# Optimization experiments

Measured on AMD Instinct MI355X. Metric: run time of the kernel, lower is better.

## Reference

```python
import jax, jax.numpy as jnp
import numpy as np

N_NODES = 10000
N_EDGES = 640000
IN_FEATS = 128
HIDDEN = 128
N_CLASSES = 64
EPS = 0.0


def _linear_params(key, fan_in, fan_out):
    k1, k2 = jax.random.split(key)
    bound = 1.0 / np.sqrt(fan_in)
    W = jax.random.uniform(k1, (fan_in, fan_out), jnp.float32, -bound, bound)
    b = jax.random.uniform(k2, (fan_out,), jnp.float32, -bound, bound)
    return W, b


def setup_inputs() -> dict:
    key = jax.random.key(0)
    ks = jax.random.split(key, 8)
    features = jax.random.normal(ks[0], (N_NODES, IN_FEATS), jnp.float32)
    src = jax.random.randint(ks[1], (N_EDGES,), 0, N_NODES, jnp.int64 if jax.config.jax_enable_x64 else jnp.int32)
    dst = jax.random.randint(ks[2], (N_EDGES,), 0, N_NODES, jnp.int64 if jax.config.jax_enable_x64 else jnp.int32)
    W1, b1 = _linear_params(ks[3], IN_FEATS, HIDDEN)
    W3, b3 = _linear_params(ks[4], HIDDEN, HIDDEN)
    W4, b4 = _linear_params(ks[5], HIDDEN, HIDDEN)
    W2, b2 = _linear_params(ks[6], HIDDEN, N_CLASSES)
    return {"features": features, "src": src, "dst": dst,
            "W1": W1, "b1": b1, "W3": W3, "b3": b3,
            "W4": W4, "b4": b4, "W2": W2, "b2": b2}


def gin_conv(h, src, dst, W, b):
    # sum-aggregate neighbor features: agg[v] = sum_{(u->v)} h[u]
    agg = jax.ops.segment_sum(h[src], dst, num_segments=N_NODES)
    z = (1.0 + EPS) * h + agg
    return z @ W + b


def reference(features, src, dst, W1, b1, W3, b3, W4, b4, W2, b2):
    h = gin_conv(features, src, dst, W1, b1)
    h = jax.nn.relu(h)
    h = gin_conv(h, src, dst, W3, b3)
    h = jax.nn.relu(h)
    h = gin_conv(h, src, dst, W4, b4)
    h = jax.nn.relu(h)
    h = gin_conv(h, src, dst, W2, b2)
    return h
```

## Files before the change

kernel.cpp:

```cpp
#include <hip/hip_runtime.h>
#include <hip/hip_bf16.h>

#define N_NODES 10000
#define N_EDGES 640000
#define FEATS   128
#define CAP     192
#define NBUCK   157
#define ECHUNK  2048
#define NPB     313
#define OSTR    160
#define TILE    8


__global__ __launch_bounds__(256) void bin_pack(const int* __restrict__ src,
                                                const int* __restrict__ dst,
                                                uint* __restrict__ bucketed,
                                                ushort* __restrict__ goffs) {
    __shared__ int hist[NBUCK];
    __shared__ int offs[NBUCK + 1];
    __shared__ int scan[256];
    __shared__ uint staging[ECHUNK];
    const int tid = threadIdx.x;
    const int b = blockIdx.x;
    const int e0 = b * ECHUNK;
    for (int i = tid; i < NBUCK; i += 256) hist[i] = 0;
    __syncthreads();
    int dreg[8];
#pragma unroll
    for (int i = 0; i < 8; ++i) {
        int e = e0 + tid + i * 256;
        dreg[i] = (e < N_EDGES) ? dst[e] : -1;
        if (dreg[i] >= 0) atomicAdd(&hist[dreg[i] >> 6], 1);
    }
    __syncthreads();
    int val = (tid < NBUCK) ? hist[tid] : 0;
    scan[tid] = val;
    __syncthreads();
    for (int off = 1; off < 256; off <<= 1) {
        int t = (tid >= off) ? scan[tid - off] : 0;
        __syncthreads();
        scan[tid] += t;
        __syncthreads();
    }
    if (tid < NBUCK) offs[tid] = scan[tid] - val;
    if (tid == 0) offs[NBUCK] = scan[NBUCK - 1];
    for (int i = tid; i < NBUCK; i += 256) hist[i] = 0;
    __syncthreads();
    if (tid <= NBUCK) goffs[b * OSTR + tid] = (ushort)offs[tid];
#pragma unroll
    for (int i = 0; i < 8; ++i) {
        int e = e0 + tid + i * 256;
        if (dreg[i] >= 0) {
            int s = src[e];
            int bk = dreg[i] >> 6;
            int slot = offs[bk] + atomicAdd(&hist[bk], 1);
            staging[slot] = ((uint)s << 6) | (uint)(dreg[i] & 63);
        }
    }
    __syncthreads();
    uint4* gu = (uint4*)(bucketed + (size_t)b * ECHUNK);
    const uint4* lu = (const uint4*)staging;
#pragma unroll
    for (int i = 0; i < ECHUNK / 4 / 256; ++i)
        gu[tid + i * 256] = lu[tid + i * 256];
}


__global__ __launch_bounds__(256) void build_ell(const uint* __restrict__ bucketed,
                                                 const ushort* __restrict__ goffs,
                                                 ushort* __restrict__ ell,
                                                 int* __restrict__ cnts) {
    __shared__ ushort lell[64 * CAP];
    __shared__ int lcur[64];
    const int tid = threadIdx.x;
    const int bk = blockIdx.x;
    if (tid < 64) lcur[tid] = 0;
    __syncthreads();
    for (int b = tid; b < NPB; b += 256) {
        int off0 = goffs[b * OSTR + bk];
        int off1 = goffs[b * OSTR + bk + 1];
        const uint* p0 = bucketed + (size_t)b * ECHUNK;
        for (int i = off0; i < off1; ++i) {
            uint p = p0[i];
            int v = p & 63;
            int slot = atomicAdd(&lcur[v], 1);
            if (slot < CAP) lell[v * CAP + slot] = (ushort)(p >> 6);
        }
    }
    __syncthreads();
    const int node0 = bk * 64;
    int nn = N_NODES - node0;
    if (nn > 64) nn = 64;
    const uint4* lu = (const uint4*)lell;
    uint4* gu = (uint4*)(ell + (size_t)node0 * CAP);
    const int nq = nn * (CAP / 8);
    for (int i = tid; i < nq; i += 256) gu[i] = lu[i];
    for (int v = tid; v < nn; v += 256) {
        int c = lcur[v];
        cnts[node0 + v] = (c > CAP) ? CAP : c;
    }
}


__global__ __launch_bounds__(256) void f2b_kernel(const float* __restrict__ in,
                                                  ushort* __restrict__ out, int n4) {
    int i = blockIdx.x * 256 + threadIdx.x;
    if (i >= n4) return;
    float4 f = ((const float4*)in)[i];
    __hip_bfloat16 b0 = __float2bfloat16(f.x);
    __hip_bfloat16 b1 = __float2bfloat16(f.y);
    __hip_bfloat16 b2 = __float2bfloat16(f.z);
    __hip_bfloat16 b3 = __float2bfloat16(f.w);
    ushort4 o;
    o.x = *(const ushort*)&b0; o.y = *(const ushort*)&b1;
    o.z = *(const ushort*)&b2; o.w = *(const ushort*)&b3;
    ((ushort4*)out)[i] = o;
}


__device__ __forceinline__ float bflo(uint p) { return __uint_as_float(p << 16); }
__device__ __forceinline__ float bfhi(uint p) { return __uint_as_float(p & 0xffff0000u); }

template <int FO, int RELU, int LAST>
__global__ __launch_bounds__(256) void fused_kernel(const ushort* __restrict__ hb,
                                                    const float* __restrict__ W,
                                                    const float* __restrict__ bias,
                                                    const int* __restrict__ cnts,
                                                    const ushort* __restrict__ ell,
                                                    ushort* __restrict__ hb_out,
                                                    float* __restrict__ f_out) {
    __shared__ float sZ[TILE][132];
    const int tile0 = blockIdx.x * TILE;
    const int tid = threadIdx.x;
    const int lane = tid & 63;
    const int wv = tid >> 6;
    const int g = lane >> 4;
    const int q = lane & 15;
    const uint4* __restrict__ hbq = (const uint4*)hb;

#pragma unroll
    for (int n = 0; n < 2; ++n) {
        const int v = tile0 + wv * 2 + n;
        int cnt = cnts[v];
        if (cnt > CAP) cnt = CAP;
        const ushort* __restrict__ row = ell + (size_t)v * CAP;
        float acc[8];
#pragma unroll
        for (int i = 0; i < 8; ++i) acc[i] = 0.f;
#pragma unroll 2
        for (int j = 0; j < cnt; j += 4) {
            uint2 iv = *(const uint2*)(row + j);
            uint word = (g & 2) ? iv.y : iv.x;
            uint u = (g & 1) ? (word >> 16) : (word & 0xffffu);
            float scale = (j + g < cnt) ? 1.0f : 0.0f;
            if (u > N_NODES - 1) u = N_NODES - 1;
            uint4 p = hbq[u * 16 + q];
            acc[0] = fmaf(bflo(p.x), scale, acc[0]);
            acc[1] = fmaf(bfhi(p.x), scale, acc[1]);
            acc[2] = fmaf(bflo(p.y), scale, acc[2]);
            acc[3] = fmaf(bfhi(p.y), scale, acc[3]);
            acc[4] = fmaf(bflo(p.z), scale, acc[4]);
            acc[5] = fmaf(bfhi(p.z), scale, acc[5]);
            acc[6] = fmaf(bflo(p.w), scale, acc[6]);
            acc[7] = fmaf(bfhi(p.w), scale, acc[7]);
        }
#pragma unroll
        for (int d = 16; d < 64; d <<= 1) {
#pragma unroll
            for (int i = 0; i < 8; ++i) acc[i] += __shfl_xor(acc[i], d);
        }
        if (g == 0) {
            uint4 p = hbq[(size_t)v * 16 + q];
            acc[0] += bflo(p.x); acc[1] += bfhi(p.x);
            acc[2] += bflo(p.y); acc[3] += bfhi(p.y);
            acc[4] += bflo(p.z); acc[5] += bfhi(p.z);
            acc[6] += bflo(p.w); acc[7] += bfhi(p.w);
            float4 a0 = {acc[0], acc[1], acc[2], acc[3]};
            float4 a1 = {acc[4], acc[5], acc[6], acc[7]};
            *(float4*)&sZ[wv * 2 + n][q * 8]     = a0;
            *(float4*)&sZ[wv * 2 + n][q * 8 + 4] = a1;
        }
    }
    __syncthreads();

    constexpr int GROUPS = 256 / FO;
    constexpr int ROWS   = TILE / GROUPS;
    const int col = tid % FO;
    const int gg  = tid / FO;
    float acc2[ROWS];
#pragma unroll
    for (int r = 0; r < ROWS; ++r) acc2[r] = 0.f;
#pragma unroll 2
    for (int k = 0; k < 128; k += 4) {
        float w0 = W[(k + 0) * FO + col];
        float w1 = W[(k + 1) * FO + col];
        float w2 = W[(k + 2) * FO + col];
        float w3 = W[(k + 3) * FO + col];
#pragma unroll
        for (int r = 0; r < ROWS; ++r) {
            float4 z = *(const float4*)&sZ[gg * ROWS + r][k];
            acc2[r] = fmaf(z.x, w0, acc2[r]);
            acc2[r] = fmaf(z.y, w1, acc2[r]);
            acc2[r] = fmaf(z.z, w2, acc2[r]);
            acc2[r] = fmaf(z.w, w3, acc2[r]);
        }
    }
    const float b = bias[col];
#pragma unroll
    for (int r = 0; r < ROWS; ++r) {
        const int vv = tile0 + gg * ROWS + r;
        float y = acc2[r] + b;
        if (RELU) y = fmaxf(y, 0.f);
        if (LAST) {
            f_out[(size_t)vv * FO + col] = y;
        } else {
            __hip_bfloat16 bv = __float2bfloat16(y);
            hb_out[(size_t)vv * FEATS + col] = *(const ushort*)&bv;
        }
    }
}


extern "C" void kernel_launch(void* const* d_in, const int* in_sizes, int n_in,
                              void* d_out, int out_size, void* d_ws, size_t ws_size,
                              hipStream_t stream) {
    const float* features = (const float*)d_in[0];
    const int*   src      = (const int*)d_in[1];
    const int*   dst      = (const int*)d_in[2];
    const float* W1 = (const float*)d_in[3];
    const float* b1 = (const float*)d_in[4];
    const float* W3 = (const float*)d_in[5];
    const float* b3 = (const float*)d_in[6];
    const float* W4 = (const float*)d_in[7];
    const float* b4 = (const float*)d_in[8];
    const float* W2 = (const float*)d_in[9];
    const float* b2 = (const float*)d_in[10];
    float* out = (float*)d_out;

    int*    cnts     = (int*)d_ws;
    ushort* goffs    = (ushort*)(cnts + 10240);
    uint*   bucketed = (uint*)(goffs + 50240);
    ushort* ell      = (ushort*)(bucketed + (size_t)NPB * ECHUNK);
    ushort* hb0      = ell + (size_t)N_NODES * CAP;
    ushort* hb1      = hb0 + (size_t)N_NODES * FEATS;

    bin_pack<<<NPB, 256, 0, stream>>>(src, dst, bucketed, goffs);
    build_ell<<<NBUCK, 256, 0, stream>>>(bucketed, goffs, ell, cnts);
    f2b_kernel<<<(N_NODES * FEATS / 4 + 255) / 256, 256, 0, stream>>>(features, hb0, N_NODES * FEATS / 4);

    const int fblocks = N_NODES / TILE;

    fused_kernel<128, 1, 0><<<fblocks, 256, 0, stream>>>(hb0, W1, b1, cnts, ell, hb1, nullptr);
    fused_kernel<128, 1, 0><<<fblocks, 256, 0, stream>>>(hb1, W3, b3, cnts, ell, hb0, nullptr);
    fused_kernel<128, 1, 0><<<fblocks, 256, 0, stream>>>(hb0, W4, b4, cnts, ell, hb1, nullptr);
    fused_kernel<64, 0, 1><<<fblocks, 256, 0, stream>>>(hb1, W2, b2, cnts, ell, nullptr, out);
}
```

Baseline: 120.7 us.

## Reorder last GIN layer as transform-then-aggregate, fold conversion into bin_pack, widen build_ell

The last layer now multiplies by W2 first, producing a 64-wide bf16 intermediate, and then aggregates neighbors in that narrower space, which halves the gather bytes for that layer. The float-to-bf16 feature conversion is merged into bin_pack to save a launch, and build_ell now uses 512 threads with wave-parallel scanning of each bucket. The trade-offs are an extra launch for the split final layer and an extra bf16 rounding of the intermediate before aggregation.

```diff
diff --git a/kernel.cpp b/kernel.cpp
--- a/kernel.cpp
+++ b/kernel.cpp
@@ -11,11 +11,16 @@
 #define OSTR    160
 #define TILE    8
 
+__device__ __forceinline__ float bflo(uint p) { return __uint_as_float(p << 16); }
+__device__ __forceinline__ float bfhi(uint p) { return __uint_as_float(p & 0xffff0000u); }
+
 
 __global__ __launch_bounds__(256) void bin_pack(const int* __restrict__ src,
                                                 const int* __restrict__ dst,
                                                 uint* __restrict__ bucketed,
-                                                ushort* __restrict__ goffs) {
+                                                ushort* __restrict__ goffs,
+                                                const float* __restrict__ features,
+                                                ushort* __restrict__ hb0) {
     __shared__ int hist[NBUCK];
     __shared__ int offs[NBUCK + 1];
     __shared__ int scan[256];
@@ -63,10 +68,23 @@
 #pragma unroll
     for (int i = 0; i < ECHUNK / 4 / 256; ++i)
         gu[tid + i * 256] = lu[tid + i * 256];
-}
-
-
-__global__ __launch_bounds__(256) void build_ell(const uint* __restrict__ bucketed,
+
+    const int n4 = N_NODES * FEATS / 4;
+    for (int i = b * 256 + tid; i < n4; i += NPB * 256) {
+        float4 f = ((const float4*)features)[i];
+        __hip_bfloat16 b0 = __float2bfloat16(f.x);
+        __hip_bfloat16 b1 = __float2bfloat16(f.y);
+        __hip_bfloat16 b2 = __float2bfloat16(f.z);
+        __hip_bfloat16 b3 = __float2bfloat16(f.w);
+        ushort4 o;
+        o.x = *(const ushort*)&b0; o.y = *(const ushort*)&b1;
+        o.z = *(const ushort*)&b2; o.w = *(const ushort*)&b3;
+        ((ushort4*)hb0)[i] = o;
+    }
+}
+
+
+__global__ __launch_bounds__(512) void build_ell(const uint* __restrict__ bucketed,
                                                  const ushort* __restrict__ goffs,
                                                  ushort* __restrict__ ell,
                                                  int* __restrict__ cnts) {
@@ -76,11 +94,13 @@
     const int bk = blockIdx.x;
     if (tid < 64) lcur[tid] = 0;
     __syncthreads();
-    for (int b = tid; b < NPB; b += 256) {
+    const int wv = tid >> 6;
+    const int lane = tid & 63;
+    for (int b = wv; b < NPB; b += 8) {
         int off0 = goffs[b * OSTR + bk];
         int off1 = goffs[b * OSTR + bk + 1];
         const uint* p0 = bucketed + (size_t)b * ECHUNK;
-        for (int i = off0; i < off1; ++i) {
+        for (int i = off0 + lane; i < off1; i += 64) {
             uint p = p0[i];
             int v = p & 63;
             int slot = atomicAdd(&lcur[v], 1);
@@ -94,41 +114,21 @@
     const uint4* lu = (const uint4*)lell;
     uint4* gu = (uint4*)(ell + (size_t)node0 * CAP);
     const int nq = nn * (CAP / 8);
-    for (int i = tid; i < nq; i += 256) gu[i] = lu[i];
-    for (int v = tid; v < nn; v += 256) {
+    for (int i = tid; i < nq; i += 512) gu[i] = lu[i];
+    for (int v = tid; v < nn; v += 512) {
         int c = lcur[v];
         cnts[node0 + v] = (c > CAP) ? CAP : c;
     }
 }
 
 
-__global__ __launch_bounds__(256) void f2b_kernel(const float* __restrict__ in,
-                                                  ushort* __restrict__ out, int n4) {
-    int i = blockIdx.x * 256 + threadIdx.x;
-    if (i >= n4) return;
-    float4 f = ((const float4*)in)[i];
-    __hip_bfloat16 b0 = __float2bfloat16(f.x);
-    __hip_bfloat16 b1 = __float2bfloat16(f.y);
-    __hip_bfloat16 b2 = __float2bfloat16(f.z);
-    __hip_bfloat16 b3 = __float2bfloat16(f.w);
-    ushort4 o;
-    o.x = *(const ushort*)&b0; o.y = *(const ushort*)&b1;
-    o.z = *(const ushort*)&b2; o.w = *(const ushort*)&b3;
-    ((ushort4*)out)[i] = o;
-}
-
-
-__device__ __forceinline__ float bflo(uint p) { return __uint_as_float(p << 16); }
-__device__ __forceinline__ float bfhi(uint p) { return __uint_as_float(p & 0xffff0000u); }
-
-template <int FO, int RELU, int LAST>
+template <int FO, int RELU>
 __global__ __launch_bounds__(256) void fused_kernel(const ushort* __restrict__ hb,
                                                     const float* __restrict__ W,
                                                     const float* __restrict__ bias,
                                                     const int* __restrict__ cnts,
                                                     const ushort* __restrict__ ell,
-                                                    ushort* __restrict__ hb_out,
-                                                    float* __restrict__ f_out) {
+                                                    ushort* __restrict__ hb_out) {
     __shared__ float sZ[TILE][132];
     const int tile0 = blockIdx.x * TILE;
     const int tid = threadIdx.x;
@@ -211,12 +211,104 @@
         const int vv = tile0 + gg * ROWS + r;
         float y = acc2[r] + b;
         if (RELU) y = fmaxf(y, 0.f);
-        if (LAST) {
-            f_out[(size_t)vv * FO + col] = y;
-        } else {
-            __hip_bfloat16 bv = __float2bfloat16(y);
-            hb_out[(size_t)vv * FEATS + col] = *(const ushort*)&bv;
-        }
+        __hip_bfloat16 bv = __float2bfloat16(y);
+        hb_out[(size_t)vv * FEATS + col] = *(const ushort*)&bv;
+    }
+}
+
+
+__global__ __launch_bounds__(256) void gemm64(const ushort* __restrict__ hb,
+                                              const float* __restrict__ W,
+                                              ushort* __restrict__ yb) {
+    __shared__ float sZ[16][132];
+    const int node0 = blockIdx.x * 16;
+    const int tid = threadIdx.x;
+    const uint* hrow = (const uint*)(hb + (size_t)node0 * 128);
+    for (int i = tid; i < 16 * 64; i += 256) {
+        uint p = hrow[i];
+        int row = i >> 6, c2 = (i & 63) * 2;
+        sZ[row][c2] = bflo(p);
+        sZ[row][c2 + 1] = bfhi(p);
+    }
+    __syncthreads();
+    const int col = tid & 63;
+    const int g = tid >> 6;
+    float acc[4] = {0.f, 0.f, 0.f, 0.f};
+#pragma unroll 2
+    for (int k = 0; k < 128; k += 4) {
+        float w0 = W[(k + 0) * 64 + col];
+        float w1 = W[(k + 1) * 64 + col];
+        float w2 = W[(k + 2) * 64 + col];
+        float w3 = W[(k + 3) * 64 + col];
+#pragma unroll
+        for (int r = 0; r < 4; ++r) {
+            float4 z = *(const float4*)&sZ[g * 4 + r][k];
+            acc[r] = fmaf(z.x, w0, acc[r]);
+            acc[r] = fmaf(z.y, w1, acc[r]);
+            acc[r] = fmaf(z.z, w2, acc[r]);
+            acc[r] = fmaf(z.w, w3, acc[r]);
+        }
+    }
+#pragma unroll
+    for (int r = 0; r < 4; ++r) {
+        __hip_bfloat16 bv = __float2bfloat16(acc[r]);
+        yb[(size_t)(node0 + g * 4 + r) * 64 + col] = *(const ushort*)&bv;
+    }
+}
+
+
+__global__ __launch_bounds__(256) void agg64(const ushort* __restrict__ yb,
+                                             const int* __restrict__ cnts,
+                                             const ushort* __restrict__ ell,
+                                             const float* __restrict__ bias,
+                                             float* __restrict__ out) {
+    const int v = blockIdx.x * 4 + (threadIdx.x >> 6);
+    const int lane = threadIdx.x & 63;
+    const int g = lane >> 3;
+    const int q = lane & 7;
+    int cnt = cnts[v];
+    if (cnt > CAP) cnt = CAP;
+    const ushort* __restrict__ row = ell + (size_t)v * CAP;
+    const uint4* __restrict__ ybq = (const uint4*)yb;
+    float acc[8];
+#pragma unroll
+    for (int i = 0; i < 8; ++i) acc[i] = 0.f;
+#pragma unroll 2
+    for (int j = 0; j < cnt; j += 8) {
+        uint4 iv = *(const uint4*)(row + j);
+        uint a = (g & 2) ? iv.y : iv.x;
+        uint b = (g & 2) ? iv.w : iv.z;
+        uint word = (g & 4) ? b : a;
+        uint u = (g & 1) ? (word >> 16) : (word & 0xffffu);
+        float scale = (j + g < cnt) ? 1.0f : 0.0f;
+        if (u > N_NODES - 1) u = N_NODES - 1;
+        uint4 p = ybq[u * 8 + q];
+        acc[0] = fmaf(bflo(p.x), scale, acc[0]);
+        acc[1] = fmaf(bfhi(p.x), scale, acc[1]);
+        acc[2] = fmaf(bflo(p.y), scale, acc[2]);
+        acc[3] = fmaf(bfhi(p.y), scale, acc[3]);
+        acc[4] = fmaf(bflo(p.z), scale, acc[4]);
+        acc[5] = fmaf(bfhi(p.z), scale, acc[5]);
+        acc[6] = fmaf(bflo(p.w), scale, acc[6]);
+        acc[7] = fmaf(bfhi(p.w), scale, acc[7]);
+    }
+#pragma unroll
+    for (int d = 8; d < 64; d <<= 1) {
+#pragma unroll
+        for (int i = 0; i < 8; ++i) acc[i] += __shfl_xor(acc[i], d);
+    }
+    if (g == 0) {
+        uint4 p = ybq[(size_t)v * 8 + q];
+        const float4* br = (const float4*)bias;
+        float4 b0 = br[q * 2], b1 = br[q * 2 + 1];
+        float4 o0, o1;
+        o0.x = acc[0] + bflo(p.x) + b0.x; o0.y = acc[1] + bfhi(p.x) + b0.y;
+        o0.z = acc[2] + bflo(p.y) + b0.z; o0.w = acc[3] + bfhi(p.y) + b0.w;
+        o1.x = acc[4] + bflo(p.z) + b1.x; o1.y = acc[5] + bfhi(p.z) + b1.y;
+        o1.z = acc[6] + bflo(p.w) + b1.z; o1.w = acc[7] + bfhi(p.w) + b1.w;
+        float4* outr = (float4*)(out + (size_t)v * 64);
+        outr[q * 2]     = o0;
+        outr[q * 2 + 1] = o1;
     }
 }
 
@@ -243,15 +335,16 @@
     ushort* ell      = (ushort*)(bucketed + (size_t)NPB * ECHUNK);
     ushort* hb0      = ell + (size_t)N_NODES * CAP;
     ushort* hb1      = hb0 + (size_t)N_NODES * FEATS;
-
-    bin_pack<<<NPB, 256, 0, stream>>>(src, dst, bucketed, goffs);
-    build_ell<<<NBUCK, 256, 0, stream>>>(bucketed, goffs, ell, cnts);
-    f2b_kernel<<<(N_NODES * FEATS / 4 + 255) / 256, 256, 0, stream>>>(features, hb0, N_NODES * FEATS / 4);
+    ushort* yb64     = hb1 + (size_t)N_NODES * FEATS;
+
+    bin_pack<<<NPB, 256, 0, stream>>>(src, dst, bucketed, goffs, features, hb0);
+    build_ell<<<NBUCK, 512, 0, stream>>>(bucketed, goffs, ell, cnts);
 
     const int fblocks = N_NODES / TILE;
 
-    fused_kernel<128, 1, 0><<<fblocks, 256, 0, stream>>>(hb0, W1, b1, cnts, ell, hb1, nullptr);
-    fused_kernel<128, 1, 0><<<fblocks, 256, 0, stream>>>(hb1, W3, b3, cnts, ell, hb0, nullptr);
-    fused_kernel<128, 1, 0><<<fblocks, 256, 0, stream>>>(hb0, W4, b4, cnts, ell, hb1, nullptr);
-    fused_kernel<64, 0, 1><<<fblocks, 256, 0, stream>>>(hb1, W2, b2, cnts, ell, nullptr, out);
-}
+    fused_kernel<128, 1><<<fblocks, 256, 0, stream>>>(hb0, W1, b1, cnts, ell, hb1);
+    fused_kernel<128, 1><<<fblocks, 256, 0, stream>>>(hb1, W3, b3, cnts, ell, hb0);
+    fused_kernel<128, 1><<<fblocks, 256, 0, stream>>>(hb0, W4, b4, cnts, ell, hb1);
+    gemm64<<<N_NODES / 16, 256, 0, stream>>>(hb1, W2, yb64);
+    agg64<<<N_NODES / 4, 256, 0, stream>>>(yb64, cnts, ell, b2, out);
+}
```

Result: slower. 130.3 us (+7.9%).
